# Kernel tuning notes

Hardware: AMD Instinct MI355X
Metric: run time of the kernel (lower is better)

Reference implementation:

```python
import jax, jax.numpy as jnp
import numpy as np

TOP_K = 2
HORIZON = 10


def _lstm_layer(seq, w_ih, w_hh, b_ih, b_hh):
    """Single torch-style LSTM layer over seq [T, in]; returns hidden seq [T, hid]."""
    hid = w_hh.shape[1]
    def step(carry, x_t):
        h, c = carry
        z = x_t @ w_ih.T + h @ w_hh.T + b_ih + b_hh  # [4*hid], torch gate order i,f,g,o
        i, f, g, o = jnp.split(z, 4)
        c = jax.nn.sigmoid(f) * c + jax.nn.sigmoid(i) * jnp.tanh(g)
        h = jax.nn.sigmoid(o) * jnp.tanh(c)
        return (h, c), h
    init = (jnp.zeros((hid,), seq.dtype), jnp.zeros((hid,), seq.dtype))
    _, hs = jax.lax.scan(step, init, seq)
    return hs


def setup_inputs() -> dict:
    key = jax.random.key(0)
    ks = jax.random.split(key, 12)
    H, E = 4096, 64
    B, S = 4, 4096
    s = 0.02
    return {
        "x": jax.random.normal(ks[0], (B, S, H), jnp.float32),
        "gate_w": jax.random.normal(ks[1], (E, H), jnp.float32) * s,
        "expert_bias": jnp.zeros((E,), jnp.float32),
        "cp_w1": jax.random.normal(ks[2], (64, H), jnp.float32) * s,
        "cp_b1": jnp.zeros((64,), jnp.float32),
        "cp_w2": jax.random.normal(ks[3], (1, 64), jnp.float32) * s,
        "cp_b2": jnp.zeros((1,), jnp.float32),
        "load_buffer": jax.random.uniform(ks[4], (50, E), jnp.float32),
        "lp_w_ih0": jax.random.normal(ks[5], (256, E), jnp.float32) * s,
        "lp_w_hh0": jax.random.normal(ks[6], (256, 64), jnp.float32) * s,
        "lp_b_ih0": jnp.zeros((256,), jnp.float32),
        "lp_b_hh0": jnp.zeros((256,), jnp.float32),
        "lp_w_ih1": jax.random.normal(ks[7], (256, 64), jnp.float32) * s,
        "lp_w_hh1": jax.random.normal(ks[8], (256, 64), jnp.float32) * s,
        "lp_b_ih1": jnp.zeros((256,), jnp.float32),
        "lp_b_hh1": jnp.zeros((256,), jnp.float32),
        "head_w": jax.random.normal(ks[9], (E * HORIZON, 64), jnp.float32) * s,
        "head_b": jnp.zeros((E * HORIZON,), jnp.float32),
    }


def reference(x, gate_w, expert_bias, cp_w1, cp_b1, cp_w2, cp_b2, load_buffer,
              lp_w_ih0, lp_w_hh0, lp_b_ih0, lp_b_hh0,
              lp_w_ih1, lp_w_hh1, lp_b_ih1, lp_b_hh1, head_w, head_b):
    sg = jax.lax.stop_gradient
    B, S, H = x.shape
    E = gate_w.shape[0]
    flat = x.reshape(-1, H)                       # [N, H]
    N = flat.shape[0]

    # --- routing logits (small gate GEMM) ---
    logits = flat @ gate_w.T                      # [N, E]

    # --- LSTM load prediction (torch.no_grad in original) ---
    seq = sg(load_buffer)
    h1 = _lstm_layer(seq, sg(lp_w_ih0), sg(lp_w_hh0), sg(lp_b_ih0), sg(lp_b_hh0))
    h2 = _lstm_layer(h1, sg(lp_w_ih1), sg(lp_w_hh1), sg(lp_b_ih1), sg(lp_b_hh1))
    pred = h2[-1] @ sg(head_w).T + sg(head_b)     # [E*HORIZON]
    future_load = jax.nn.softmax(pred.reshape(E, HORIZON).mean(axis=1))  # [E]

    # --- bias + predicted-load adjustment, softmax, top-k ---
    adj_logits = logits + expert_bias - sg(future_load)
    probs = jax.nn.softmax(adj_logits, axis=-1)   # [N, E]
    top_scores, top_idx = jax.lax.top_k(probs, TOP_K)
    top_scores = top_scores / top_scores.sum(axis=-1, keepdims=True)

    # --- switch-style load-balancing auxiliary loss ---
    one_hot = jax.nn.one_hot(top_idx, E, dtype=probs.dtype)   # [N, k, E]
    f = one_hot.sum(axis=(0, 1)) / (N * TOP_K)                # routed fraction per expert
    P = probs.mean(axis=0)                                    # mean routing prob
    aux_loss = E * jnp.sum(f * P)

    # --- dynamic capacity from complexity predictor (torch.no_grad) ---
    comp = jax.nn.sigmoid(
        jax.nn.relu(flat @ sg(cp_w1).T + sg(cp_b1)) @ sg(cp_w2).T + sg(cp_b2))  # [N,1]
    capacity = jnp.clip(0.5 + 1.5 * comp.mean(), 0.5, 2.0)

    return top_scores, top_idx, aux_loss, capacity, future_load
```

## Files before the change

kernel.cpp:

```cpp
#include <hip/hip_runtime.h>
#include <stdint.h>

#define IMG_OFF_BYTES 80000
#define CHUNK_IMG 20480
#define LOGITS_OFF 680000
#define TAU 1e-3f

#define BUF_STRIDE 30720
#define BOFF 10240
#define XLOFF 5120
#define WLOFF 10240

typedef __attribute__((ext_vector_type(8))) short short8v;
typedef __attribute__((ext_vector_type(4))) short short4v;
typedef __attribute__((ext_vector_type(4))) float f32x4;

__device__ __forceinline__ float rlf(float v, int l) {
  return __int_as_float(__builtin_amdgcn_readlane(__float_as_int(v), l));
}
__device__ __forceinline__ float wsum(float v) {
#pragma unroll
  for (int o = 32; o; o >>= 1) v += __shfl_xor(v, o, 64);
  return v;
}
__device__ __forceinline__ float wmax(float v) {
#pragma unroll
  for (int o = 32; o; o >>= 1) v = fmaxf(v, __shfl_xor(v, o, 64));
  return v;
}
__device__ __forceinline__ unsigned short f2bf(float f) {
  unsigned u = __float_as_uint(f);
  u += 0x7fffu + ((u >> 16) & 1u);
  return (unsigned short)(u >> 16);
}
__device__ __forceinline__ float bf2f(unsigned short h) {
  return __uint_as_float(((unsigned)h) << 16);
}
__device__ __forceinline__ short8v frag8(const char* p0, const char* p1) {
  short4v a = *(const short4v*)p0;
  short4v b = *(const short4v*)p1;
  return __builtin_shufflevector(a, b, 0, 1, 2, 3, 4, 5, 6, 7);
}

__global__ __launch_bounds__(256) void prep_kernel(
    const float* __restrict__ gate_w, const float* __restrict__ cp_w1,
    float* __restrict__ ws)
{
  const int c = blockIdx.x;
  const int tid = threadIdx.x;
  if (c == 0 && tid < 144) ws[64 + tid] = 0.f;
  const int row = tid >> 1;
  const int half = tid & 1;
  const float* src = (row < 64) ? (gate_w + (size_t)row * 4096)
                                : (cp_w1 + (size_t)(row - 64) * 4096);
  float v[16];
#pragma unroll
  for (int j = 0; j < 4; ++j)
    *(float4*)&v[j * 4] = *(const float4*)(src + c * 32 + half * 16 + j * 4);
  uint4 hv, lv;
  unsigned hu[8], lu[8];
#pragma unroll
  for (int i = 0; i < 8; ++i) {
    unsigned short h0 = f2bf(v[2 * i]), h1 = f2bf(v[2 * i + 1]);
    unsigned short l0 = f2bf(v[2 * i] - bf2f(h0));
    unsigned short l1 = f2bf(v[2 * i + 1] - bf2f(h1));
    hu[i] = (unsigned)h0 | ((unsigned)h1 << 16);
    lu[i] = (unsigned)l0 | ((unsigned)l1 << 16);
  }
  char* img = (char*)ws + IMG_OFF_BYTES + (size_t)c * CHUNK_IMG;
  hv.x = hu[0]; hv.y = hu[1]; hv.z = hu[2]; hv.w = hu[3];
  *(uint4*)(img + row * 80 + half * 32) = hv;
  hv.x = hu[4]; hv.y = hu[5]; hv.z = hu[6]; hv.w = hu[7];
  *(uint4*)(img + row * 80 + half * 32 + 16) = hv;
  lv.x = lu[0]; lv.y = lu[1]; lv.z = lu[2]; lv.w = lu[3];
  *(uint4*)(img + WLOFF + row * 80 + half * 32) = lv;
  lv.x = lu[4]; lv.y = lu[5]; lv.z = lu[6]; lv.w = lu[7];
  *(uint4*)(img + WLOFF + row * 80 + half * 32 + 16) = lv;
}

__device__ void lstm_device(
    char* ldsbase,
    const float* __restrict__ lb,
    const float* __restrict__ wih0, const float* __restrict__ whh0,
    const float* __restrict__ bih0, const float* __restrict__ bhh0,
    const float* __restrict__ wih1, const float* __restrict__ whh1,
    const float* __restrict__ bih1, const float* __restrict__ bhh1,
    const float* __restrict__ head_w, const float* __restrict__ head_b,
    float* __restrict__ ws, float* __restrict__ out, int N)
{
  float* seqh = (float*)ldsbase;
  float* h1s  = seqh + 3200;
  float* zbuf = h1s + 3200;
  float* hbuf = zbuf + 256;
  float* preds = hbuf + 64;
  const int tid = threadIdx.x;
  const int lane = tid & 63;
  for (int i = tid; i < 3200; i += 256) seqh[i] = lb[i];

  float hv = 0.f;
#pragma unroll 1
  for (int L = 0; L < 2; ++L) {
    const float* wip  = L ? wih1 : wih0;
    const float* whp  = L ? whh1 : whh0;
    const float* bip  = L ? bih1 : bih0;
    const float* bhp  = L ? bhh1 : bhh0;
    const float* seqp = L ? h1s  : seqh;
    float wiR[64], whR[64];
#pragma unroll
    for (int j = 0; j < 64; j += 4) {
      *(float4*)&wiR[j] = *(const float4*)(wip + tid * 64 + j);
      *(float4*)&whR[j] = *(const float4*)(whp + tid * 64 + j);
    }
    const float bsum = bip[tid] + bhp[tid];
    float c_reg = 0.f;
    hv = 0.f;
    if (tid < 64) hbuf[tid] = 0.f;
    __syncthreads();
#pragma unroll 1
    for (int t = 0; t < 50; ++t) {
      const float xv = seqp[t * 64 + lane];
      float a0 = bsum, a1 = 0.f, a2 = 0.f, a3 = 0.f;
#pragma unroll
      for (int j = 0; j < 64; j += 4) {
        a0 = fmaf(rlf(xv, j + 0), wiR[j + 0], a0);
        a1 = fmaf(rlf(xv, j + 1), wiR[j + 1], a1);
        a2 = fmaf(rlf(xv, j + 2), wiR[j + 2], a2);
        a3 = fmaf(rlf(xv, j + 3), wiR[j + 3], a3);
      }
#pragma unroll
      for (int j = 0; j < 64; j += 4) {
        a0 = fmaf(rlf(hv, j + 0), whR[j + 0], a0);
        a1 = fmaf(rlf(hv, j + 1), whR[j + 1], a1);
        a2 = fmaf(rlf(hv, j + 2), whR[j + 2], a2);
        a3 = fmaf(rlf(hv, j + 3), whR[j + 3], a3);
      }
      zbuf[tid] = (a0 + a1) + (a2 + a3);
      __syncthreads();
      if (tid < 64) {
        const float zi = zbuf[tid], zf = zbuf[64 + tid];
        const float zg = zbuf[128 + tid], zo = zbuf[192 + tid];
        const float si = 1.f / (1.f + expf(-zi));
        const float sf = 1.f / (1.f + expf(-zf));
        const float so = 1.f / (1.f + expf(-zo));
        c_reg = sf * c_reg + si * tanhf(zg);
        const float h = so * tanhf(c_reg);
        hbuf[tid] = h;
        if (L == 0) h1s[t * 64 + tid] = h;
      }
      __syncthreads();
      hv = hbuf[lane];
    }
    __syncthreads();
  }
  for (int o = tid; o < 640; o += 256) {
    const float* hw = head_w + o * 64;
    float a0 = 0.f, a1 = 0.f, a2 = 0.f, a3 = 0.f;
#pragma unroll
    for (int j = 0; j < 64; j += 4) {
      a0 = fmaf(rlf(hv, j + 0), hw[j + 0], a0);
      a1 = fmaf(rlf(hv, j + 1), hw[j + 1], a1);
      a2 = fmaf(rlf(hv, j + 2), hw[j + 2], a2);
      a3 = fmaf(rlf(hv, j + 3), hw[j + 3], a3);
    }
    preds[o] = (a0 + a1) + (a2 + a3) + head_b[o];
  }
  __syncthreads();
  if (tid < 64) {
    float m = 0.f;
#pragma unroll
    for (int h = 0; h < 10; ++h) m += preds[tid * 10 + h];
    m = m / 10.f;
    const float mx = wmax(m);
    const float p = expf(m - mx);
    const float s = wsum(p);
    const float flv = p / s;
    ws[tid] = flv;
    out[4 * N + 2 + tid] = flv;
  }
}

__global__ __launch_bounds__(256) void gemm_kernel(
    const float* __restrict__ x, float* __restrict__ ws, float* __restrict__ out,
    const float* __restrict__ lb,
    const float* __restrict__ wih0, const float* __restrict__ whh0,
    const float* __restrict__ bih0, const float* __restrict__ bhh0,
    const float* __restrict__ wih1, const float* __restrict__ whh1,
    const float* __restrict__ bih1, const float* __restrict__ bhh1,
    const float* __restrict__ head_w, const float* __restrict__ head_b,
    int N)
{
  __shared__ __align__(16) char lds[61440];
  if (blockIdx.x == 256) {
    lstm_device(lds, lb, wih0, whh0, bih0, bhh0, wih1, whh1, bih1, bhh1,
                head_w, head_b, ws, out, N);
    return;
  }
  const int tid = threadIdx.x;
  const int lane = tid & 63;
  const int wv = __builtin_amdgcn_readfirstlane(tid >> 6);
  const int tb = blockIdx.x * 64;
  const int r15 = lane & 15;
  const int fo = (lane >> 4) * 8;
  const int row = tid >> 2;
  const int kslot = tid & 3;
  const float* xsrc = x + (size_t)(tb + row) * 4096 + kslot * 8;
  const char* wimg = (const char*)ws + IMG_OFF_BYTES;
  char* buf0 = lds;
  char* buf1 = lds + BUF_STRIDE;

  f32x4 acc[4][2];
#pragma unroll
  for (int mi = 0; mi < 4; ++mi)
#pragma unroll
    for (int ni = 0; ni < 2; ++ni) acc[mi][ni] = (f32x4)0.f;

  float xa[8], xb[8];

#define LOADX(R, C)                                                        \
  { *(float4*)&R[0] = *(const float4*)(xsrc + (size_t)(C) * 32);           \
    *(float4*)&R[4] = *(const float4*)(xsrc + (size_t)(C) * 32 + 4); }

#define WRITEX(R, BASE)                                                    \
  { uint4 hv, lv; unsigned hu[4], lu[4];                                   \
    _Pragma("unroll")                                                      \
    for (int i = 0; i < 4; ++i) {                                          \
      unsigned short h0 = f2bf(R[2 * i]), h1 = f2bf(R[2 * i + 1]);         \
      unsigned short l0 = f2bf(R[2 * i] - bf2f(h0));                       \
      unsigned short l1 = f2bf(R[2 * i + 1] - bf2f(h1));                   \
      hu[i] = (unsigned)h0 | ((unsigned)h1 << 16);                         \
      lu[i] = (unsigned)l0 | ((unsigned)l1 << 16);                         \
    }                                                                      \
    hv.x = hu[0]; hv.y = hu[1]; hv.z = hu[2]; hv.w = hu[3];                \
    lv.x = lu[0]; lv.y = lu[1]; lv.z = lu[2]; lv.w = lu[3];                \
    *(uint4*)((BASE) + row * 80 + kslot * 16) = hv;                        \
    *(uint4*)((BASE) + XLOFF + row * 80 + kslot * 16) = lv; }

#define STAGEB(C, BASE)                                                    \
  { const char* s = wimg + (size_t)(C) * CHUNK_IMG + (wv * 5) * 1024 +     \
                    lane * 16;                                             \
    char* d = (BASE) + BOFF + (wv * 5) * 1024;                             \
    _Pragma("unroll")                                                      \
    for (int i = 0; i < 5; ++i)                                            \
      __builtin_amdgcn_global_load_lds(                                    \
          (const __attribute__((address_space(1))) uint32_t*)(s + i * 1024), \
          (__attribute__((address_space(3))) uint32_t*)(d + i * 1024),     \
          16, 0, 0); }

#define COMPUTE(BASE)                                                      \
  { const char* bA = (BASE);                                               \
    const char* bB = (BASE) + BOFF;                                        \
    short8v xh[4], xl[4], wh[2], wl[2];                                    \
    _Pragma("unroll")                                                      \
    for (int mi = 0; mi < 4; ++mi) {                                       \
      const char* p = bA + (mi * 16 + r15) * 80 + fo;                      \
      xh[mi] = frag8(p, p + 32);                                           \
      xl[mi] = frag8(p + XLOFF, p + XLOFF + 32);                           \
    }                                                                      \
    _Pragma("unroll")                                                      \
    for (int ni = 0; ni < 2; ++ni) {                                       \
      const char* p = bB + (wv * 32 + ni * 16 + r15) * 80 + fo;            \
      wh[ni] = frag8(p, p + 32);                                           \
      wl[ni] = frag8(p + WLOFF, p + WLOFF + 32);                           \
    }                                                                      \
    _Pragma("unroll")                                                      \
    for (int mi = 0; mi < 4; ++mi)                                         \
      _Pragma("unroll")                                                    \
      for (int ni = 0; ni < 2; ++ni) {                                     \
        acc[mi][ni] = __builtin_amdgcn_mfma_f32_16x16x32_bf16(             \
            xh[mi], wh[ni], acc[mi][ni], 0, 0, 0);                         \
        acc[mi][ni] = __builtin_amdgcn_mfma_f32_16x16x32_bf16(             \
            xh[mi], wl[ni], acc[mi][ni], 0, 0, 0);                         \
        acc[mi][ni] = __builtin_amdgcn_mfma_f32_16x16x32_bf16(             \
            xl[mi], wh[ni], acc[mi][ni], 0, 0, 0);                         \
      } }

  LOADX(xa, 0);
  LOADX(xb, 1);
  STAGEB(0, buf0);
  WRITEX(xa, buf0);
  __syncthreads();

#pragma unroll 1
  for (int cc = 0; cc < 64; ++cc) {
    const int c0 = 2 * cc, c1 = 2 * cc + 1;
    STAGEB(c0 + 1, buf1);
    if (c0 + 2 < 128) LOADX(xa, c0 + 2);
    COMPUTE(buf0);
    WRITEX(xb, buf1);
    __syncthreads();
    if (c1 + 1 < 128) STAGEB(c1 + 1, buf0);
    if (c1 + 2 < 128) LOADX(xb, c1 + 2);
    COMPUTE(buf1);
    if (c1 + 1 < 128) WRITEX(xa, buf0);
    __syncthreads();
  }

  float* lg = ws + LOGITS_OFF;
#pragma unroll
  for (int mi = 0; mi < 4; ++mi)
#pragma unroll
    for (int ni = 0; ni < 2; ++ni)
#pragma unroll
      for (int r = 0; r < 4; ++r) {
        const int tokrow = tb + mi * 16 + (lane >> 4) * 4 + r;
        const int col = wv * 32 + ni * 16 + r15;
        lg[(size_t)tokrow * 128 + col] = acc[mi][ni][r];
      }
#undef LOADX
#undef WRITEX
#undef STAGEB
#undef COMPUTE
}

__global__ __launch_bounds__(256) void epi_kernel(
    const float* __restrict__ eb_p, const float* __restrict__ cp_b1,
    const float* __restrict__ cp_w2, const float* __restrict__ cp_b2,
    float* __restrict__ ws, float* __restrict__ out, int N)
{
  const int tid = threadIdx.x;
  const int lane = tid & 63;
  const int wv = __builtin_amdgcn_readfirstlane(tid >> 6);
  const int tb = blockIdx.x * 64;
  const float* lg = ws + LOGITS_OFF;
  int* qd = (int*)(ws + 200);
  __shared__ float sP[64];
  __shared__ float scnt[64];
  __shared__ float scomp;
  if (tid < 64) { sP[tid] = 0.f; scnt[tid] = 0.f; }
  if (tid == 0) scomp = 0.f;
  __syncthreads();

  const float eb = eb_p[lane];
  const float fl = ws[lane];
  const float cb1 = cp_b1[lane];
  const float cw2 = cp_w2[lane];
  const float cb2 = cp_b2[0];
  float psum_local = 0.f, comp_local = 0.f;
  float* o_ts = out;
  float* o_ti = out + 2 * N;

#pragma unroll 1
  for (int tt = 0; tt < 16; ++tt) {
    const int tok = tb + wv * 16 + tt;
    const float lgv = lg[(size_t)tok * 128 + lane];
    const float lc  = lg[(size_t)tok * 128 + 64 + lane];
    float rr = fmaxf(lc + cb1, 0.f) * cw2;
    rr = wsum(rr);
    const float comp = 1.f / (1.f + expf(-(rr + cb2)));
    comp_local += comp;
    const float a = lgv + eb - fl;
    float m1 = a; int i1 = lane;
#pragma unroll
    for (int o = 32; o; o >>= 1) {
      const float ov = __shfl_xor(m1, o, 64);
      const int oi = __shfl_xor(i1, o, 64);
      if (ov > m1 || (ov == m1 && oi < i1)) { m1 = ov; i1 = oi; }
    }
    float m2 = (lane == i1) ? -1e30f : a; int i2 = lane;
#pragma unroll
    for (int o = 32; o; o >>= 1) {
      const float ov = __shfl_xor(m2, o, 64);
      const int oi = __shfl_xor(i2, o, 64);
      if (ov > m2 || (ov == m2 && oi < i2)) { m2 = ov; i2 = oi; }
    }
    float m3 = (lane == i1 || lane == i2) ? -1e30f : a;
#pragma unroll
    for (int o = 32; o; o >>= 1) m3 = fmaxf(m3, __shfl_xor(m3, o, 64));
    const float p = expf(a - m1);
    const float ssum = wsum(p);
    const float prob = p / ssum;
    psum_local += prob;
    const float s1 = rlf(prob, i1);
    const float s2 = rlf(prob, i2);
    if (lane == 0) {
      const float inv = 1.f / (s1 + s2);
      o_ts[tok * 2 + 0] = s1 * inv;
      o_ts[tok * 2 + 1] = s2 * inv;
      o_ti[tok * 2 + 0] = (float)i1;
      o_ti[tok * 2 + 1] = (float)i2;
      atomicAdd(&scnt[i1], 1.f);
      atomicAdd(&scnt[i2], 1.f);
      if (m1 - m2 < TAU || m2 - m3 < TAU) {
        int slot = atomicAdd(qd, 1);
        qd[8 + slot] = tok;
      }
    }
  }
  atomicAdd(&sP[lane], psum_local);
  if (lane == 0) atomicAdd(&scomp, comp_local);
  __syncthreads();
  if (tid < 64) {
    atomicAdd(&ws[64 + tid], sP[tid]);
    atomicAdd(&ws[128 + tid], scnt[tid]);
  }
  if (tid == 0) atomicAdd(&ws[192], scomp);
}

__global__ __launch_bounds__(256) void repair_kernel(
    const float* __restrict__ x, const float* __restrict__ gate_w,
    const float* __restrict__ eb_p, float* __restrict__ ws,
    float* __restrict__ out, int N)
{
  const int tid = threadIdx.x;
  __shared__ float red[256];
  int* qd = (int*)(ws + 200);
  const int qn = qd[0];
  float* o_ts = out;
  float* o_ti = out + 2 * N;

  for (int e = blockIdx.x; e < qn; e += gridDim.x) {
    const int tok = qd[8 + e];
    const int o = tid & 63;
    const int kq = tid >> 6;
    const float* xr = x + (size_t)tok * 4096 + kq * 1024;
    const float* wr = gate_w + (size_t)o * 4096 + kq * 1024;
    float s = 0.f;
#pragma unroll 4
    for (int j = 0; j < 256; ++j) {
      const float4 xv = *(const float4*)(xr + j * 4);
      const float4 wv = *(const float4*)(wr + j * 4);
      s = fmaf(xv.x, wv.x, s); s = fmaf(xv.y, wv.y, s);
      s = fmaf(xv.z, wv.z, s); s = fmaf(xv.w, wv.w, s);
    }
    red[tid] = s;
    __syncthreads();
    if (tid < 64) {
      const float a = red[tid] + red[64 + tid] + red[128 + tid] +
                      red[192 + tid] + eb_p[tid] - ws[tid];
      const int lane = tid;
      float m1 = a; int i1 = lane;
#pragma unroll
      for (int oo = 32; oo; oo >>= 1) {
        const float ov = __shfl_xor(m1, oo, 64);
        const int oi = __shfl_xor(i1, oo, 64);
        if (ov > m1 || (ov == m1 && oi < i1)) { m1 = ov; i1 = oi; }
      }
      float m2 = (lane == i1) ? -1e30f : a; int i2 = lane;
#pragma unroll
      for (int oo = 32; oo; oo >>= 1) {
        const float ov = __shfl_xor(m2, oo, 64);
        const int oi = __shfl_xor(i2, oo, 64);
        if (ov > m2 || (ov == m2 && oi < i2)) { m2 = ov; i2 = oi; }
      }
      const float p = expf(a - m1);
      const float ssum = wsum(p);
      const float s1 = rlf(p, i1) / ssum;
      const float s2 = rlf(p, i2) / ssum;
      if (lane == 0) {
        const int i1o = (int)o_ti[tok * 2 + 0];
        const int i2o = (int)o_ti[tok * 2 + 1];
        const float inv = 1.f / (s1 + s2);
        o_ts[tok * 2 + 0] = s1 * inv;
        o_ts[tok * 2 + 1] = s2 * inv;
        o_ti[tok * 2 + 0] = (float)i1;
        o_ti[tok * 2 + 1] = (float)i2;
        if (i1o != i1 || i2o != i2) {
          atomicAdd(&ws[128 + i1o], -1.f);
          atomicAdd(&ws[128 + i2o], -1.f);
          atomicAdd(&ws[128 + i1], 1.f);
          atomicAdd(&ws[128 + i2], 1.f);
        }
      }
    }
    __syncthreads();
  }
}

__global__ __launch_bounds__(64) void fin_kernel(const float* __restrict__ ws,
                                                 float* __restrict__ out, int N) {
  const int e = threadIdx.x;
  const float P = ws[64 + e] / (float)N;
  const float f = ws[128 + e] / (float)(2 * N);
  const float v = wsum(f * P);
  if (e == 0) {
    out[4 * N + 0] = 64.f * v;
    float cap = 0.5f + 1.5f * (ws[192] / (float)N);
    out[4 * N + 1] = fminf(fmaxf(cap, 0.5f), 2.f);
  }
}

extern "C" void kernel_launch(void* const* d_in, const int* in_sizes, int n_in,
                              void* d_out, int out_size, void* d_ws, size_t ws_size,
                              hipStream_t stream) {
  const float* x          = (const float*)d_in[0];
  const float* gate_w     = (const float*)d_in[1];
  const float* expert_bias= (const float*)d_in[2];
  const float* cp_w1      = (const float*)d_in[3];
  const float* cp_b1      = (const float*)d_in[4];
  const float* cp_w2      = (const float*)d_in[5];
  const float* cp_b2      = (const float*)d_in[6];
  const float* load_buffer= (const float*)d_in[7];
  const float* wih0       = (const float*)d_in[8];
  const float* whh0       = (const float*)d_in[9];
  const float* bih0       = (const float*)d_in[10];
  const float* bhh0       = (const float*)d_in[11];
  const float* wih1       = (const float*)d_in[12];
  const float* whh1       = (const float*)d_in[13];
  const float* bih1       = (const float*)d_in[14];
  const float* bhh1       = (const float*)d_in[15];
  const float* head_w     = (const float*)d_in[16];
  const float* head_b     = (const float*)d_in[17];
  float* out = (float*)d_out;
  float* ws  = (float*)d_ws;
  const int N = in_sizes[0] / 4096;

  prep_kernel<<<128, 256, 0, stream>>>(gate_w, cp_w1, ws);
  gemm_kernel<<<N / 64 + 1, 256, 0, stream>>>(x, ws, out, load_buffer,
                                              wih0, whh0, bih0, bhh0,
                                              wih1, whh1, bih1, bhh1,
                                              head_w, head_b, N);
  epi_kernel<<<N / 64, 256, 0, stream>>>(expert_bias, cp_b1, cp_w2, cp_b2,
                                         ws, out, N);
  repair_kernel<<<128, 256, 0, stream>>>(x, gate_w, expert_bias, ws, out, N);
  fin_kernel<<<1, 64, 0, stream>>>(ws, out, N);
}
```

Before: 227.4 us.

## Halve GEMM token tile to 32 rows and pre-swizzle weight image for direct fragment loads

The GEMM block now covers 32 tokens instead of 64, doubling the grid to 512 compute blocks so more of the GPU's CUs are busy on the memory-bound x stream. The prep kernel writes the weight image in an interleaved layout so each lane can read its B fragment with one 16-byte LDS load instead of two 8-byte pieces. The LDS footprint shrinks to two 25.6KB buffers, and the epilogue kernel is resized to match. In exchange, each block re-stages the full weight chunk for half as many tokens, doubling total weight traffic through L2.

```diff
diff --git a/kernel.cpp b/kernel.cpp
--- a/kernel.cpp
+++ b/kernel.cpp
@@ -3,13 +3,14 @@
 
 #define IMG_OFF_BYTES 80000
 #define CHUNK_IMG 20480
+#define IMG_LO 10240
 #define LOGITS_OFF 680000
 #define TAU 1e-3f
 
-#define BUF_STRIDE 30720
-#define BOFF 10240
-#define XLOFF 5120
-#define WLOFF 10240
+#define XH 0
+#define XL 2560
+#define WH 5120
+#define BUF_STRIDE 25600
 
 typedef __attribute__((ext_vector_type(8))) short short8v;
 typedef __attribute__((ext_vector_type(4))) short short4v;
@@ -57,25 +58,23 @@
 #pragma unroll
   for (int j = 0; j < 4; ++j)
     *(float4*)&v[j * 4] = *(const float4*)(src + c * 32 + half * 16 + j * 4);
-  uint4 hv, lv;
-  unsigned hu[8], lu[8];
-#pragma unroll
-  for (int i = 0; i < 8; ++i) {
-    unsigned short h0 = f2bf(v[2 * i]), h1 = f2bf(v[2 * i + 1]);
-    unsigned short l0 = f2bf(v[2 * i] - bf2f(h0));
-    unsigned short l1 = f2bf(v[2 * i + 1] - bf2f(h1));
-    hu[i] = (unsigned)h0 | ((unsigned)h1 << 16);
-    lu[i] = (unsigned)l0 | ((unsigned)l1 << 16);
-  }
   char* img = (char*)ws + IMG_OFF_BYTES + (size_t)c * CHUNK_IMG;
-  hv.x = hu[0]; hv.y = hu[1]; hv.z = hu[2]; hv.w = hu[3];
-  *(uint4*)(img + row * 80 + half * 32) = hv;
-  hv.x = hu[4]; hv.y = hu[5]; hv.z = hu[6]; hv.w = hu[7];
-  *(uint4*)(img + row * 80 + half * 32 + 16) = hv;
-  lv.x = lu[0]; lv.y = lu[1]; lv.z = lu[2]; lv.w = lu[3];
-  *(uint4*)(img + WLOFF + row * 80 + half * 32) = lv;
-  lv.x = lu[4]; lv.y = lu[5]; lv.z = lu[6]; lv.w = lu[7];
-  *(uint4*)(img + WLOFF + row * 80 + half * 32 + 16) = lv;
+#pragma unroll
+  for (int i = 0; i < 4; ++i) {
+    unsigned short h0 = f2bf(v[4 * i + 0]), h1 = f2bf(v[4 * i + 1]);
+    unsigned short h2 = f2bf(v[4 * i + 2]), h3 = f2bf(v[4 * i + 3]);
+    unsigned short l0 = f2bf(v[4 * i + 0] - bf2f(h0));
+    unsigned short l1 = f2bf(v[4 * i + 1] - bf2f(h1));
+    unsigned short l2 = f2bf(v[4 * i + 2] - bf2f(h2));
+    unsigned short l3 = f2bf(v[4 * i + 3] - bf2f(h3));
+    uint2 hv, lv;
+    hv.x = (unsigned)h0 | ((unsigned)h1 << 16);
+    hv.y = (unsigned)h2 | ((unsigned)h3 << 16);
+    lv.x = (unsigned)l0 | ((unsigned)l1 << 16);
+    lv.y = (unsigned)l2 | ((unsigned)l3 << 16);
+    *(uint2*)(img + row * 80 + i * 16 + half * 8) = hv;
+    *(uint2*)(img + IMG_LO + row * 80 + i * 16 + half * 8) = lv;
+  }
 }
 
 __device__ void lstm_device(
@@ -189,8 +188,8 @@
     const float* __restrict__ head_w, const float* __restrict__ head_b,
     int N)
 {
-  __shared__ __align__(16) char lds[61440];
-  if (blockIdx.x == 256) {
+  __shared__ __align__(16) char lds[2 * BUF_STRIDE];
+  if (blockIdx.x == 512) {
     lstm_device(lds, lb, wih0, whh0, bih0, bhh0, wih1, whh1, bih1, bhh1,
                 head_w, head_b, ws, out, N);
     return;
@@ -198,80 +197,74 @@
   const int tid = threadIdx.x;
   const int lane = tid & 63;
   const int wv = __builtin_amdgcn_readfirstlane(tid >> 6);
-  const int tb = blockIdx.x * 64;
+  const int tb = blockIdx.x * 32;
   const int r15 = lane & 15;
-  const int fo = (lane >> 4) * 8;
-  const int row = tid >> 2;
-  const int kslot = tid & 3;
-  const float* xsrc = x + (size_t)(tb + row) * 4096 + kslot * 8;
+  const int q = lane >> 4;
+  const int row = tid >> 3;
+  const int kslot = tid & 7;
+  const float* xsrc = x + (size_t)(tb + row) * 4096 + kslot * 4;
   const char* wimg = (const char*)ws + IMG_OFF_BYTES;
   char* buf0 = lds;
   char* buf1 = lds + BUF_STRIDE;
 
-  f32x4 acc[4][2];
-#pragma unroll
-  for (int mi = 0; mi < 4; ++mi)
+  f32x4 acc[2][2];
+#pragma unroll
+  for (int mi = 0; mi < 2; ++mi)
 #pragma unroll
     for (int ni = 0; ni < 2; ++ni) acc[mi][ni] = (f32x4)0.f;
 
-  float xa[8], xb[8];
-
-#define LOADX(R, C)                                                        \
-  { *(float4*)&R[0] = *(const float4*)(xsrc + (size_t)(C) * 32);           \
-    *(float4*)&R[4] = *(const float4*)(xsrc + (size_t)(C) * 32 + 4); }
-
-#define WRITEX(R, BASE)                                                    \
-  { uint4 hv, lv; unsigned hu[4], lu[4];                                   \
-    _Pragma("unroll")                                                      \
-    for (int i = 0; i < 4; ++i) {                                          \
-      unsigned short h0 = f2bf(R[2 * i]), h1 = f2bf(R[2 * i + 1]);         \
-      unsigned short l0 = f2bf(R[2 * i] - bf2f(h0));                       \
-      unsigned short l1 = f2bf(R[2 * i + 1] - bf2f(h1));                   \
-      hu[i] = (unsigned)h0 | ((unsigned)h1 << 16);                         \
-      lu[i] = (unsigned)l0 | ((unsigned)l1 << 16);                         \
-    }                                                                      \
-    hv.x = hu[0]; hv.y = hu[1]; hv.z = hu[2]; hv.w = hu[3];                \
-    lv.x = lu[0]; lv.y = lu[1]; lv.z = lu[2]; lv.w = lu[3];                \
-    *(uint4*)((BASE) + row * 80 + kslot * 16) = hv;                        \
-    *(uint4*)((BASE) + XLOFF + row * 80 + kslot * 16) = lv; }
-
-#define STAGEB(C, BASE)                                                    \
-  { const char* s = wimg + (size_t)(C) * CHUNK_IMG + (wv * 5) * 1024 +     \
-                    lane * 16;                                             \
-    char* d = (BASE) + BOFF + (wv * 5) * 1024;                             \
-    _Pragma("unroll")                                                      \
-    for (int i = 0; i < 5; ++i)                                            \
-      __builtin_amdgcn_global_load_lds(                                    \
-          (const __attribute__((address_space(1))) uint32_t*)(s + i * 1024), \
-          (__attribute__((address_space(3))) uint32_t*)(d + i * 1024),     \
+  float4 xa, xb;
+
+#define LOADX(R, C) { R = *(const float4*)(xsrc + (size_t)(C) * 32); }
+
+#define WRITEX(R, BASE)                                                     \
+  { unsigned short h0 = f2bf(R.x), h1 = f2bf(R.y);                          \
+    unsigned short h2 = f2bf(R.z), h3 = f2bf(R.w);                          \
+    unsigned short l0 = f2bf(R.x - bf2f(h0)), l1 = f2bf(R.y - bf2f(h1));    \
+    unsigned short l2 = f2bf(R.z - bf2f(h2)), l3 = f2bf(R.w - bf2f(h3));    \
+    uint2 hv, lv;                                                           \
+    hv.x = (unsigned)h0 | ((unsigned)h1 << 16);                             \
+    hv.y = (unsigned)h2 | ((unsigned)h3 << 16);                             \
+    lv.x = (unsigned)l0 | ((unsigned)l1 << 16);                             \
+    lv.y = (unsigned)l2 | ((unsigned)l3 << 16);                             \
+    *(uint2*)((BASE) + XH + row * 80 + kslot * 8) = hv;                     \
+    *(uint2*)((BASE) + XL + row * 80 + kslot * 8) = lv; }
+
+#define STAGEB(C, BASE)                                                     \
+  { const char* s = wimg + (size_t)(C) * CHUNK_IMG + wv * 5120 + lane * 16; \
+    char* d = (BASE) + WH + wv * 5120;                                      \
+    _Pragma("unroll")                                                       \
+    for (int i = 0; i < 5; ++i)                                             \
+      __builtin_amdgcn_global_load_lds(                                     \
+          (const __attribute__((address_space(1))) uint32_t*)(s + i * 1024),\
+          (__attribute__((address_space(3))) uint32_t*)(d + i * 1024),      \
           16, 0, 0); }
 
-#define COMPUTE(BASE)                                                      \
-  { const char* bA = (BASE);                                               \
-    const char* bB = (BASE) + BOFF;                                        \
-    short8v xh[4], xl[4], wh[2], wl[2];                                    \
-    _Pragma("unroll")                                                      \
-    for (int mi = 0; mi < 4; ++mi) {                                       \
-      const char* p = bA + (mi * 16 + r15) * 80 + fo;                      \
-      xh[mi] = frag8(p, p + 32);                                           \
-      xl[mi] = frag8(p + XLOFF, p + XLOFF + 32);                           \
-    }                                                                      \
-    _Pragma("unroll")                                                      \
-    for (int ni = 0; ni < 2; ++ni) {                                       \
-      const char* p = bB + (wv * 32 + ni * 16 + r15) * 80 + fo;            \
-      wh[ni] = frag8(p, p + 32);                                           \
-      wl[ni] = frag8(p + WLOFF, p + WLOFF + 32);                           \
-    }                                                                      \
-    _Pragma("unroll")                                                      \
-    for (int mi = 0; mi < 4; ++mi)                                         \
-      _Pragma("unroll")                                                    \
-      for (int ni = 0; ni < 2; ++ni) {                                     \
-        acc[mi][ni] = __builtin_amdgcn_mfma_f32_16x16x32_bf16(             \
-            xh[mi], wh[ni], acc[mi][ni], 0, 0, 0);                         \
-        acc[mi][ni] = __builtin_amdgcn_mfma_f32_16x16x32_bf16(             \
-            xh[mi], wl[ni], acc[mi][ni], 0, 0, 0);                         \
-        acc[mi][ni] = __builtin_amdgcn_mfma_f32_16x16x32_bf16(             \
-            xl[mi], wh[ni], acc[mi][ni], 0, 0, 0);                         \
+#define COMPUTE(BASE)                                                       \
+  { short8v xh[2], xl[2], wh[2], wl[2];                                     \
+    _Pragma("unroll")                                                       \
+    for (int mi = 0; mi < 2; ++mi) {                                        \
+      const char* p = (BASE) + XH + (mi * 16 + r15) * 80 + q * 8;           \
+      xh[mi] = frag8(p, p + 32);                                            \
+      const char* p2 = (BASE) + XL + (mi * 16 + r15) * 80 + q * 8;          \
+      xl[mi] = frag8(p2, p2 + 32);                                          \
+    }                                                                       \
+    _Pragma("unroll")                                                       \
+    for (int ni = 0; ni < 2; ++ni) {                                        \
+      const char* pw = (BASE) + WH + (wv * 32 + ni * 16 + r15) * 80 + q * 16;\
+      wh[ni] = *(const short8v*)pw;                                         \
+      wl[ni] = *(const short8v*)(pw + IMG_LO);                              \
+    }                                                                       \
+    _Pragma("unroll")                                                       \
+    for (int mi = 0; mi < 2; ++mi)                                          \
+      _Pragma("unroll")                                                     \
+      for (int ni = 0; ni < 2; ++ni) {                                      \
+        acc[mi][ni] = __builtin_amdgcn_mfma_f32_16x16x32_bf16(              \
+            xh[mi], wh[ni], acc[mi][ni], 0, 0, 0);                          \
+        acc[mi][ni] = __builtin_amdgcn_mfma_f32_16x16x32_bf16(              \
+            xh[mi], wl[ni], acc[mi][ni], 0, 0, 0);                          \
+        acc[mi][ni] = __builtin_amdgcn_mfma_f32_16x16x32_bf16(              \
+            xl[mi], wh[ni], acc[mi][ni], 0, 0, 0);                          \
       } }
 
   LOADX(xa, 0);
@@ -297,12 +290,12 @@
 
   float* lg = ws + LOGITS_OFF;
 #pragma unroll
-  for (int mi = 0; mi < 4; ++mi)
+  for (int mi = 0; mi < 2; ++mi)
 #pragma unroll
     for (int ni = 0; ni < 2; ++ni)
 #pragma unroll
       for (int r = 0; r < 4; ++r) {
-        const int tokrow = tb + mi * 16 + (lane >> 4) * 4 + r;
+        const int tokrow = tb + mi * 16 + q * 4 + r;
         const int col = wv * 32 + ni * 16 + r15;
         lg[(size_t)tokrow * 128 + col] = acc[mi][ni][r];
       }
@@ -320,7 +313,7 @@
   const int tid = threadIdx.x;
   const int lane = tid & 63;
   const int wv = __builtin_amdgcn_readfirstlane(tid >> 6);
-  const int tb = blockIdx.x * 64;
+  const int tb = blockIdx.x * 32;
   const float* lg = ws + LOGITS_OFF;
   int* qd = (int*)(ws + 200);
   __shared__ float sP[64];
@@ -340,8 +333,8 @@
   float* o_ti = out + 2 * N;
 
 #pragma unroll 1
-  for (int tt = 0; tt < 16; ++tt) {
-    const int tok = tb + wv * 16 + tt;
+  for (int tt = 0; tt < 8; ++tt) {
+    const int tok = tb + wv * 8 + tt;
     const float lgv = lg[(size_t)tok * 128 + lane];
     const float lc  = lg[(size_t)tok * 128 + 64 + lane];
     float rr = fmaxf(lc + cb1, 0.f) * cw2;
@@ -505,11 +498,11 @@
   const int N = in_sizes[0] / 4096;
 
   prep_kernel<<<128, 256, 0, stream>>>(gate_w, cp_w1, ws);
-  gemm_kernel<<<N / 64 + 1, 256, 0, stream>>>(x, ws, out, load_buffer,
+  gemm_kernel<<<N / 32 + 1, 256, 0, stream>>>(x, ws, out, load_buffer,
                                               wih0, whh0, bih0, bhh0,
                                               wih1, whh1, bih1, bhh1,
                                               head_w, head_b, N);
-  epi_kernel<<<N / 64, 256, 0, stream>>>(expert_bias, cp_b1, cp_w2, cp_b2,
+  epi_kernel<<<N / 32, 256, 0, stream>>>(expert_bias, cp_b1, cp_w2, cp_b2,
                                          ws, out, N);
   repair_kernel<<<128, 256, 0, stream>>>(x, gate_w, expert_bias, ws, out, N);
   fin_kernel<<<1, 64, 0, stream>>>(ws, out, N);
```

Result: slower. 280.0 us (+23.1%).

## Split GEMM K dimension across two blocks with atomic accumulation

Applied to the files above, without the earlier changes.

The logits GEMM now splits the 4096-wide reduction into two halves handled by separate blocks, launching 512 GEMM blocks plus the LSTM block (moved to block 0 so it starts first). Partial results are combined with atomicAdd into a logits buffer that prep_kernel now zero-fills. The epilogue kernel is also launched with twice as many blocks, each handling 32 tokens. The goal is to fill more of the GPU's compute units, since 256 blocks underuse the device. The cost is extra zeroing writes and atomic traffic, and float atomics make the summation order nondeterministic.

```diff
diff --git a/kernel.cpp b/kernel.cpp
--- a/kernel.cpp
+++ b/kernel.cpp
@@ -49,6 +49,12 @@
   const int c = blockIdx.x;
   const int tid = threadIdx.x;
   if (c == 0 && tid < 144) ws[64 + tid] = 0.f;
+  {
+    float4 z = make_float4(0.f, 0.f, 0.f, 0.f);
+    float4* lz = (float4*)(ws + LOGITS_OFF + c * 16384);
+#pragma unroll
+    for (int i = 0; i < 16; ++i) lz[tid + i * 256] = z;
+  }
   const int row = tid >> 1;
   const int half = tid & 1;
   const float* src = (row < 64) ? (gate_w + (size_t)row * 4096)
@@ -190,15 +196,17 @@
     int N)
 {
   __shared__ __align__(16) char lds[61440];
-  if (blockIdx.x == 256) {
+  if (blockIdx.x == 0) {
     lstm_device(lds, lb, wih0, whh0, bih0, bhh0, wih1, whh1, bih1, bhh1,
                 head_w, head_b, ws, out, N);
     return;
   }
+  const int b = blockIdx.x - 1;
+  const int tb = (b & 255) * 64;
+  const int ck0 = (b >> 8) * 64;
   const int tid = threadIdx.x;
   const int lane = tid & 63;
   const int wv = __builtin_amdgcn_readfirstlane(tid >> 6);
-  const int tb = blockIdx.x * 64;
   const int r15 = lane & 15;
   const int fo = (lane >> 4) * 8;
   const int row = tid >> 2;
@@ -274,24 +282,24 @@
             xl[mi], wh[ni], acc[mi][ni], 0, 0, 0);                         \
       } }
 
-  LOADX(xa, 0);
-  LOADX(xb, 1);
-  STAGEB(0, buf0);
+  LOADX(xa, ck0);
+  LOADX(xb, ck0 + 1);
+  STAGEB(ck0, buf0);
   WRITEX(xa, buf0);
   __syncthreads();
 
 #pragma unroll 1
-  for (int cc = 0; cc < 64; ++cc) {
-    const int c0 = 2 * cc, c1 = 2 * cc + 1;
+  for (int cc = 0; cc < 32; ++cc) {
+    const int c0 = ck0 + 2 * cc, c1 = c0 + 1;
     STAGEB(c0 + 1, buf1);
-    if (c0 + 2 < 128) LOADX(xa, c0 + 2);
+    if (cc < 31) LOADX(xa, c0 + 2);
     COMPUTE(buf0);
     WRITEX(xb, buf1);
     __syncthreads();
-    if (c1 + 1 < 128) STAGEB(c1 + 1, buf0);
-    if (c1 + 2 < 128) LOADX(xb, c1 + 2);
+    if (cc < 31) STAGEB(c1 + 1, buf0);
+    if (cc < 31) LOADX(xb, c1 + 2);
     COMPUTE(buf1);
-    if (c1 + 1 < 128) WRITEX(xa, buf0);
+    if (cc < 31) WRITEX(xa, buf0);
     __syncthreads();
   }
 
@@ -304,7 +312,7 @@
       for (int r = 0; r < 4; ++r) {
         const int tokrow = tb + mi * 16 + (lane >> 4) * 4 + r;
         const int col = wv * 32 + ni * 16 + r15;
-        lg[(size_t)tokrow * 128 + col] = acc[mi][ni][r];
+        atomicAdd(&lg[(size_t)tokrow * 128 + col], acc[mi][ni][r]);
       }
 #undef LOADX
 #undef WRITEX
@@ -320,7 +328,7 @@
   const int tid = threadIdx.x;
   const int lane = tid & 63;
   const int wv = __builtin_amdgcn_readfirstlane(tid >> 6);
-  const int tb = blockIdx.x * 64;
+  const int tb = blockIdx.x * 32;
   const float* lg = ws + LOGITS_OFF;
   int* qd = (int*)(ws + 200);
   __shared__ float sP[64];
@@ -340,8 +348,8 @@
   float* o_ti = out + 2 * N;
 
 #pragma unroll 1
-  for (int tt = 0; tt < 16; ++tt) {
-    const int tok = tb + wv * 16 + tt;
+  for (int tt = 0; tt < 8; ++tt) {
+    const int tok = tb + wv * 8 + tt;
     const float lgv = lg[(size_t)tok * 128 + lane];
     const float lc  = lg[(size_t)tok * 128 + 64 + lane];
     float rr = fmaxf(lc + cb1, 0.f) * cw2;
@@ -505,11 +513,11 @@
   const int N = in_sizes[0] / 4096;
 
   prep_kernel<<<128, 256, 0, stream>>>(gate_w, cp_w1, ws);
-  gemm_kernel<<<N / 64 + 1, 256, 0, stream>>>(x, ws, out, load_buffer,
-                                              wih0, whh0, bih0, bhh0,
-                                              wih1, whh1, bih1, bhh1,
-                                              head_w, head_b, N);
-  epi_kernel<<<N / 64, 256, 0, stream>>>(expert_bias, cp_b1, cp_w2, cp_b2,
+  gemm_kernel<<<513, 256, 0, stream>>>(x, ws, out, load_buffer,
+                                       wih0, whh0, bih0, bhh0,
+                                       wih1, whh1, bih1, bhh1,
+                                       head_w, head_b, N);
+  epi_kernel<<<N / 32, 256, 0, stream>>>(expert_bias, cp_b1, cp_w2, cp_b2,
                                          ws, out, N);
   repair_kernel<<<128, 256, 0, stream>>>(x, gate_w, expert_bias, ws, out, N);
   fin_kernel<<<1, 64, 0, stream>>>(ws, out, N);
```

Result: no change. 224.4 us (-1.3%).
